# Optimization experiments

Measured on AMD Instinct MI355X. Metric: run time of the kernel, lower is better.

The kernel has to match this reference:

```python
import jax, jax.numpy as jnp
import numpy as np

B, T, D, H = 4, 4096, 1024, 64

def setup_inputs() -> dict:
    key = jax.random.key(0)
    k1, k2, k3, k4 = jax.random.split(key, 4)
    x = jax.random.normal(k1, (B, T, D), dtype=jnp.float32)
    Wk = jax.random.normal(k2, (D, H), dtype=jnp.float32) * (D ** -0.5)
    Wq = jax.random.normal(k3, (D, H), dtype=jnp.float32) * (D ** -0.5)
    Wv = jax.random.normal(k4, (D, H), dtype=jnp.float32) * (D ** -0.5)
    return {"x": x, "Wk": Wk, "Wq": Wq, "Wv": Wv}

def reference(x, Wk, Wq, Wv):
    # single-head causal self-attention (dropout inactive: training=False)
    k = x @ Wk  # [B,T,H]
    q = x @ Wq  # [B,T,H]
    v = x @ Wv  # [B,T,H]
    scale = jnp.float32(1.0) / jnp.sqrt(jnp.float32(H))
    wei = jnp.einsum('bth,bsh->bts', q, k) * scale  # [B,T,T]
    t = x.shape[1]
    causal = jnp.tril(jnp.ones((t, t), dtype=bool))[None, :, :]
    wei = jnp.where(causal, wei, jnp.float32(-jnp.inf))
    wei = jax.nn.softmax(wei, axis=-1)
    out = jnp.einsum('bts,bsh->bth', wei, v)  # [B,T,H]
    return out
```

## Files before the change

### kernel.cpp

```cpp
#include <hip/hip_runtime.h>

typedef __bf16 bf16_t;
typedef __bf16 bf16x8 __attribute__((ext_vector_type(8)));
typedef __bf16 bf16x4 __attribute__((ext_vector_type(4)));
typedef float  f32x4  __attribute__((ext_vector_type(4)));
typedef float  f32x16 __attribute__((ext_vector_type(16)));

#define B_  4
#define T_  4096
#define H_  64
#define BT  (B_*T_)

#define QSCALE 0.1803368801111204f

#define NSLOT_PB 1088
#define NSLOT    4352

#define WS_KFR  0x0000000u
#define WS_QFR  0x0200000u
#define WS_VFR  0x0400000u
#define WS_WTF  0x0600000u
#define WS_POUT 0x0680000u
#define WS_PL   0x1780000u

#define MFMA16(a,b,c) __builtin_amdgcn_mfma_f32_16x16x32_bf16((a),(b),(c),0,0,0)
#define MFMA32(a,b,c) __builtin_amdgcn_mfma_f32_32x32x16_bf16((a),(b),(c),0,0,0)

__device__ __forceinline__ unsigned pk2(float a, float b) {
  union { __bf16 h[2]; unsigned u; } u_;
  u_.h[0] = (__bf16)a; u_.h[1] = (__bf16)b;
  return u_.u;
}

__device__ __forceinline__ f32x16 zero16() {
  f32x16 z;
#pragma unroll
  for (int i = 0; i < 16; ++i) z[i] = 0.f;
  return z;
}

__global__ __launch_bounds__(128) void wtrans_kernel(
    const float* __restrict__ Wk, const float* __restrict__ Wq,
    const float* __restrict__ Wv, bf16_t* __restrict__ WTf) {
  __shared__ float lw[64][17];
  int bid = blockIdx.x;
  int nt = bid >> 4;
  int kc = bid & 15;
  int w  = nt >> 2;
  const float* W = (w == 0) ? Wk : (w == 1) ? Wq : Wv;
  float sc = (w == 1) ? QSCALE : 1.0f;
  int nl0 = (nt & 3) * 16;

  int t = threadIdx.x;
  int rr = t >> 1;
  int c0 = (t & 1) * 8;
  const float* src = W + (size_t)(kc*64 + rr)*64 + nl0 + c0;
  float4 v0 = *reinterpret_cast<const float4*>(src);
  float4 v1 = *reinterpret_cast<const float4*>(src + 4);
  lw[rr][c0+0] = v0.x; lw[rr][c0+1] = v0.y; lw[rr][c0+2] = v0.z; lw[rr][c0+3] = v0.w;
  lw[rr][c0+4] = v1.x; lw[rr][c0+5] = v1.y; lw[rr][c0+6] = v1.z; lw[rr][c0+7] = v1.w;
  __syncthreads();

  int kk   = t >> 6;
  int lane = t & 63;
  int col  = lane & 15;
  int g    = lane >> 4;
  bf16x8 o;
#pragma unroll
  for (int e = 0; e < 8; ++e) o[e] = (bf16_t)(lw[kk*32 + g*8 + e][col] * sc);
  *reinterpret_cast<bf16x8*>(WTf + ((size_t)bid*2 + kk)*512 + lane*8) = o;
}

__global__ __launch_bounds__(256) void proj_kernel(
    const float* __restrict__ x, const bf16_t* __restrict__ WTf,
    bf16_t* __restrict__ kfr, bf16_t* __restrict__ qfr, bf16_t* __restrict__ vfr) {
  __shared__ __bf16 xs[2][16][72];
  int tid  = threadIdx.x;
  int wv   = tid >> 6;
  int lane = tid & 63;
  int col  = lane & 15;
  int g    = lane >> 4;
  int m0   = blockIdx.x * 16;

  f32x4 zero4 = {0.f, 0.f, 0.f, 0.f};
  f32x4 acc[3] = {zero4, zero4, zero4};

  int srow = tid >> 4;
  int scol = (tid & 15) * 4;
  const float* xrow = x + (size_t)(m0 + srow)*1024 + scol;

  float4 a0 = *reinterpret_cast<const float4*>(xrow);
  float4 b0 = *reinterpret_cast<const float4*>(xrow + 64);
  {
    bf16x4 pk = { (bf16_t)a0.x,(bf16_t)a0.y,(bf16_t)a0.z,(bf16_t)a0.w };
    *reinterpret_cast<bf16x4*>(&xs[0][srow][scol]) = pk;
  }

  const bf16_t* wtb = WTf + lane*8;

  for (int t = 0; t < 16; ++t) {
    __syncthreads();
    int cur = t & 1;
    if (t + 2 < 16) {
      const float* p = xrow + (t+2)*64;
      if ((t & 1) == 0) a0 = *reinterpret_cast<const float4*>(p);
      else              b0 = *reinterpret_cast<const float4*>(p);
    }
#pragma unroll
    for (int kk = 0; kk < 2; ++kk) {
      int ko = kk*32 + g*8;
      bf16x8 f0 = *(const bf16x8*)&xs[cur][col][ko];
#pragma unroll
      for (int nti = 0; nti < 3; ++nti) {
        int nt = wv*3 + nti;
        bf16x8 bfr = *(const bf16x8*)(wtb + ((size_t)(nt*16 + t)*2 + kk)*512);
        acc[nti] = MFMA16(f0, bfr, acc[nti]);
      }
    }
    if (t + 1 < 16) {
      float4 sv = ((t & 1) == 0) ? b0 : a0;
      bf16x4 pk = { (bf16_t)sv.x,(bf16_t)sv.y,(bf16_t)sv.z,(bf16_t)sv.w };
      *reinterpret_cast<bf16x4*>(&xs[cur^1][srow][scol]) = pk;
    }
  }
  int row0 = m0 + 4*g;
#pragma unroll
  for (int nti = 0; nti < 3; ++nti) {
    int n = wv*48 + nti*16 + col;
    f32x4 v = acc[nti];
    if (n < 128) {
      int h = n & 63;
      bf16_t* base = (n < 64) ? kfr : qfr;
#pragma unroll
      for (int r = 0; r < 4; ++r) {
        int t2 = row0 + r;
        size_t idx = (size_t)((t2>>6)*8 + ((t2>>5)&1)*4 + (h>>4))*512
                   + (size_t)((t2&31) + ((h>>3)&1)*32)*8 + (h&7);
        base[idx] = (bf16_t)v[r];
      }
    } else {
      int h = n - 128;
      size_t idx = (size_t)((row0>>6)*8 + ((h>>5)&1)*4 + ((row0>>4)&3))*512
                 + (size_t)((h&31) + ((row0>>3)&1)*32)*8 + (row0&7);
      bf16x4 pk = { (bf16_t)v[0], (bf16_t)v[1], (bf16_t)v[2], (bf16_t)v[3] };
      *reinterpret_cast<bf16x4*>(&vfr[idx]) = pk;
    }
  }
}

__global__ __launch_bounds__(64) void attn_kernel(
    const bf16_t* __restrict__ qfr, const bf16_t* __restrict__ kfr,
    const bf16_t* __restrict__ vfr, bf16_t* __restrict__ pout,
    float* __restrict__ pl) {
  int l  = threadIdx.x;
  int ql = l & 31;
  int hi = l >> 5;

  int bidx = blockIdx.x;
  int b = bidx / NSLOT_PB;
  int s = bidx - b * NSLOT_PB;
  s = NSLOT_PB - 1 - s;
  int a = 0;
#pragma unroll
  for (int aa = 1; aa < 16; ++aa) if (4*aa*(aa+1) <= s) a = aa;
  int r2 = s - 4*a*(a+1);
  int qd = r2 / (a+1);
  int c  = r2 - qd*(a+1);
  int jt = 8*a + qd;
  int slot = b*NSLOT_PB + s;

  int q0    = jt << 5;
  int kv_lo = c << 8;
  int kv_hi = min(kv_lo + 256, q0 + 32);
  int ntiles = (kv_hi - kv_lo + 63) >> 6;
  int qg = q0 + ql;

  const bf16_t* qb = qfr + (size_t)((b*T_ + q0) >> 6)*4096
                   + (size_t)((q0 >> 5) & 1)*2048 + l*8;
  bf16x8 qf0 = *(const bf16x8*)(qb);
  bf16x8 qf1 = *(const bf16x8*)(qb + 512);
  bf16x8 qf2 = *(const bf16x8*)(qb + 1024);
  bf16x8 qf3 = *(const bf16x8*)(qb + 1536);

  const bf16_t* kfb = kfr + (size_t)(b*T_)*64 + l*8;
  const bf16_t* vfb = vfr + (size_t)(b*T_)*64 + l*8;

  bf16x8 kA0,kA1,kA2,kA3, kB0,kB1,kB2,kB3;
#define LOADK(kvt_) do { const bf16_t* kp_ = kfb + (size_t)(kvt_)*64;          \
    kA0=*(const bf16x8*)(kp_);        kA1=*(const bf16x8*)(kp_+512);           \
    kA2=*(const bf16x8*)(kp_+1024);   kA3=*(const bf16x8*)(kp_+1536);          \
    kB0=*(const bf16x8*)(kp_+2048);   kB1=*(const bf16x8*)(kp_+2560);          \
    kB2=*(const bf16x8*)(kp_+3072);   kB3=*(const bf16x8*)(kp_+3584); } while(0)

  LOADK(kv_lo);

  f32x16 oA = zero16(), oB = zero16();
  float l_ = 0.f;

  for (int t = 0; t < ntiles; ++t) {
    int kvt = kv_lo + t*64;
    const bf16_t* vp = vfb + (size_t)kvt*64;
    bf16x8 vA0 = *(const bf16x8*)(vp);
    bf16x8 vA1 = *(const bf16x8*)(vp + 512);
    bf16x8 vA2 = *(const bf16x8*)(vp + 1024);
    bf16x8 vA3 = *(const bf16x8*)(vp + 1536);
    bf16x8 vB0 = *(const bf16x8*)(vp + 2048);
    bf16x8 vB1 = *(const bf16x8*)(vp + 2560);
    bf16x8 vB2 = *(const bf16x8*)(vp + 3072);
    bf16x8 vB3 = *(const bf16x8*)(vp + 3584);

    f32x16 sA = zero16(), sB = zero16();
    __builtin_amdgcn_s_setprio(1);
    sA = MFMA32(kA0, qf0, sA); sB = MFMA32(kB0, qf0, sB);
    sA = MFMA32(kA1, qf1, sA); sB = MFMA32(kB1, qf1, sB);
    sA = MFMA32(kA2, qf2, sA); sB = MFMA32(kB2, qf2, sB);
    sA = MFMA32(kA3, qf3, sA); sB = MFMA32(kB3, qf3, sB);
    __builtin_amdgcn_s_setprio(0);

    if (t + 1 < ntiles) LOADK(kvt + 64);

    if (kvt + 63 > q0) {
#pragma unroll
      for (int r = 0; r < 16; ++r) {
        int kvo = kvt + (r&3) + 8*(r>>2) + 4*hi;
        if (kvo > qg)      sA[r] = -1e30f;
        if (kvo + 32 > qg) sB[r] = -1e30f;
      }
    }

    float pA[16], pB[16];
    float ts = 0.f;
#pragma unroll
    for (int r = 0; r < 16; ++r) { pA[r] = exp2f(sA[r]); ts += pA[r]; }
#pragma unroll
    for (int r = 0; r < 16; ++r) { pB[r] = exp2f(sB[r]); ts += pB[r]; }
    l_ += ts + __shfl_xor(ts, 32);

    bf16x8 p0, p1, p2, p3;
#define MKSLICES(P, F0, F1) do {                                               \
    unsigned w0 = pk2(P[0],P[1]),   w1 = pk2(P[2],P[3]);                       \
    unsigned w2 = pk2(P[4],P[5]),   w3 = pk2(P[6],P[7]);                       \
    unsigned w4 = pk2(P[8],P[9]),   w5 = pk2(P[10],P[11]);                     \
    unsigned w6 = pk2(P[12],P[13]), w7 = pk2(P[14],P[15]);                     \
    unsigned x0 = (unsigned)__shfl_xor((int)w0,32);                            \
    unsigned x1 = (unsigned)__shfl_xor((int)w1,32);                            \
    unsigned x2 = (unsigned)__shfl_xor((int)w2,32);                            \
    unsigned x3 = (unsigned)__shfl_xor((int)w3,32);                            \
    unsigned x4 = (unsigned)__shfl_xor((int)w4,32);                            \
    unsigned x5 = (unsigned)__shfl_xor((int)w5,32);                            \
    unsigned x6 = (unsigned)__shfl_xor((int)w6,32);                            \
    unsigned x7 = (unsigned)__shfl_xor((int)w7,32);                            \
    union { unsigned d[4]; bf16x8 v; } u0_, u1_;                               \
    u0_.d[0] = hi ? x2 : w0;  u0_.d[1] = hi ? x3 : w1;                         \
    u0_.d[2] = hi ? w2 : x0;  u0_.d[3] = hi ? w3 : x1;                         \
    u1_.d[0] = hi ? x6 : w4;  u1_.d[1] = hi ? x7 : w5;                         \
    u1_.d[2] = hi ? w6 : x4;  u1_.d[3] = hi ? w7 : x5;                         \
    F0 = u0_.v; F1 = u1_.v; } while(0)
    MKSLICES(pA, p0, p1);
    MKSLICES(pB, p2, p3);

    __builtin_amdgcn_s_setprio(1);
    oA = MFMA32(vA0, p0, oA); oB = MFMA32(vB0, p0, oB);
    oA = MFMA32(vA1, p1, oA); oB = MFMA32(vB1, p1, oB);
    oA = MFMA32(vA2, p2, oA); oB = MFMA32(vB2, p2, oB);
    oA = MFMA32(vA3, p3, oA); oB = MFMA32(vB3, p3, oB);
    __builtin_amdgcn_s_setprio(0);
  }

  bf16_t* po = pout + (size_t)slot * 2048;
#pragma unroll
  for (int r = 0; r < 16; ++r) {
    int h = (r&3) + 8*(r>>2) + 4*hi;
    po[h*32 + ql]      = (bf16_t)oA[r];
    po[(h+32)*32 + ql] = (bf16_t)oB[r];
  }
  if (l < 32) pl[(size_t)slot*32 + l] = l_;
}

__global__ __launch_bounds__(256) void combine_kernel(
    const bf16_t* __restrict__ pout, const float* __restrict__ pl,
    float* __restrict__ out) {
  int blk = blockIdx.x;
  int b  = blk >> 7;
  int jt = blk & 127;
  int tid = threadIdx.x;
  int wv = tid >> 6;
  int l  = tid & 63;
  int a  = jt >> 3;
  int nch = a + 1;
  int slot0 = b*NSLOT_PB + 4*a*(a+1) + (jt & 7)*(a+1);

  float oacc[8], lacc[8];
#pragma unroll
  for (int q = 0; q < 8; ++q) { oacc[q] = 0.f; lacc[q] = 0.f; }
  for (int c2 = 0; c2 < nch; ++c2) {
    const bf16_t* pp = pout + (size_t)(slot0 + c2)*2048 + l*32 + wv*8;
    bf16x8 o8 = *(const bf16x8*)pp;
    const float* plc = pl + (size_t)(slot0 + c2)*32 + wv*8;
#pragma unroll
    for (int q = 0; q < 8; ++q) { oacc[q] += (float)o8[q]; lacc[q] += plc[q]; }
  }
  float* op = out + ((size_t)b*T_ + (size_t)jt*32 + wv*8)*64 + l;
#pragma unroll
  for (int q = 0; q < 8; ++q) op[(size_t)q*64] = oacc[q] / lacc[q];
}

extern "C" void kernel_launch(void* const* d_in, const int* in_sizes, int n_in,
                              void* d_out, int out_size, void* d_ws, size_t ws_size,
                              hipStream_t stream) {
  (void)in_sizes; (void)n_in; (void)out_size; (void)ws_size;
  const float* x  = (const float*)d_in[0];
  const float* Wk = (const float*)d_in[1];
  const float* Wq = (const float*)d_in[2];
  const float* Wv = (const float*)d_in[3];
  char* ws = (char*)d_ws;
  bf16_t* kfr  = (bf16_t*)(ws + WS_KFR);
  bf16_t* qfr  = (bf16_t*)(ws + WS_QFR);
  bf16_t* vfr  = (bf16_t*)(ws + WS_VFR);
  bf16_t* WTf  = (bf16_t*)(ws + WS_WTF);
  bf16_t* pout = (bf16_t*)(ws + WS_POUT);
  float*  pl   = (float*)(ws + WS_PL);
  float*  outp = (float*)d_out;

  hipLaunchKernelGGL(wtrans_kernel,  dim3(192),   dim3(128), 0, stream, Wk, Wq, Wv, WTf);
  hipLaunchKernelGGL(proj_kernel,    dim3(1024),  dim3(256), 0, stream, x, WTf, kfr, qfr, vfr);
  hipLaunchKernelGGL(attn_kernel,    dim3(NSLOT), dim3(64),  0, stream, qfr, kfr, vfr, pout, pl);
  hipLaunchKernelGGL(combine_kernel, dim3(512),   dim3(256), 0, stream, pout, pl, outp);
}
```

Measured before the change: 65.57 us.

## Drop LDS staging in projection, load x directly into MFMA fragments with 32-row tiles

The projection kernel no longer stages x through shared memory with barriers. Each lane now loads its own fp32 x fragment from global memory, converts it to bf16 in registers, and feeds it to the MFMA. Each block covers 32 rows instead of 16, so every weight fragment is reused for two M-tiles, and the grid is halved. Loads are software-pipelined with even/odd register sets. The cost is that all four waves read x redundantly, relying on cache, and register pressure goes up.

```diff
diff --git a/kernel.cpp b/kernel.cpp
--- a/kernel.cpp
+++ b/kernel.cpp
@@ -74,76 +74,95 @@
 __global__ __launch_bounds__(256) void proj_kernel(
     const float* __restrict__ x, const bf16_t* __restrict__ WTf,
     bf16_t* __restrict__ kfr, bf16_t* __restrict__ qfr, bf16_t* __restrict__ vfr) {
-  __shared__ __bf16 xs[2][16][72];
   int tid  = threadIdx.x;
   int wv   = tid >> 6;
   int lane = tid & 63;
   int col  = lane & 15;
   int g    = lane >> 4;
-  int m0   = blockIdx.x * 16;
-
-  f32x4 zero4 = {0.f, 0.f, 0.f, 0.f};
-  f32x4 acc[3] = {zero4, zero4, zero4};
-
-  int srow = tid >> 4;
-  int scol = (tid & 15) * 4;
-  const float* xrow = x + (size_t)(m0 + srow)*1024 + scol;
-
-  float4 a0 = *reinterpret_cast<const float4*>(xrow);
-  float4 b0 = *reinterpret_cast<const float4*>(xrow + 64);
-  {
-    bf16x4 pk = { (bf16_t)a0.x,(bf16_t)a0.y,(bf16_t)a0.z,(bf16_t)a0.w };
-    *reinterpret_cast<bf16x4*>(&xs[0][srow][scol]) = pk;
-  }
-
-  const bf16_t* wtb = WTf + lane*8;
-
-  for (int t = 0; t < 16; ++t) {
-    __syncthreads();
-    int cur = t & 1;
-    if (t + 2 < 16) {
-      const float* p = xrow + (t+2)*64;
-      if ((t & 1) == 0) a0 = *reinterpret_cast<const float4*>(p);
-      else              b0 = *reinterpret_cast<const float4*>(p);
+  int m0   = blockIdx.x * 32;
+
+  f32x4 acc00 = {0.f,0.f,0.f,0.f}, acc01 = acc00, acc02 = acc00;
+  f32x4 acc10 = acc00, acc11 = acc00, acc12 = acc00;
+
+  const float*  xpA = x + (size_t)(m0 + col)*1024 + g*8;
+  const float*  xpB = xpA + (size_t)16*1024;
+  const bf16_t* wtb = WTf + (size_t)(wv*3)*32*512 + lane*8;
+
+  float4 aE0 = *(const float4*)(xpA);      float4 aE1 = *(const float4*)(xpA + 4);
+  float4 aE2 = *(const float4*)(xpB);      float4 aE3 = *(const float4*)(xpB + 4);
+  bf16x8 bE0 = *(const bf16x8*)(wtb + (size_t)(0*32 + 0)*512);
+  bf16x8 bE1 = *(const bf16x8*)(wtb + (size_t)(1*32 + 0)*512);
+  bf16x8 bE2 = *(const bf16x8*)(wtb + (size_t)(2*32 + 0)*512);
+  float4 aO0 = *(const float4*)(xpA + 32); float4 aO1 = *(const float4*)(xpA + 36);
+  float4 aO2 = *(const float4*)(xpB + 32); float4 aO3 = *(const float4*)(xpB + 36);
+  bf16x8 bO0 = *(const bf16x8*)(wtb + (size_t)(0*32 + 1)*512);
+  bf16x8 bO1 = *(const bf16x8*)(wtb + (size_t)(1*32 + 1)*512);
+  bf16x8 bO2 = *(const bf16x8*)(wtb + (size_t)(2*32 + 1)*512);
+
+  for (int u = 0; u < 16; ++u) {
+    {
+      bf16x8 af0 = { (bf16_t)aE0.x,(bf16_t)aE0.y,(bf16_t)aE0.z,(bf16_t)aE0.w,
+                     (bf16_t)aE1.x,(bf16_t)aE1.y,(bf16_t)aE1.z,(bf16_t)aE1.w };
+      bf16x8 af1 = { (bf16_t)aE2.x,(bf16_t)aE2.y,(bf16_t)aE2.z,(bf16_t)aE2.w,
+                     (bf16_t)aE3.x,(bf16_t)aE3.y,(bf16_t)aE3.z,(bf16_t)aE3.w };
+      bf16x8 b0 = bE0, b1 = bE1, b2 = bE2;
+      if (u < 15) {
+        int jn = 2*u + 2;
+        aE0 = *(const float4*)(xpA + jn*32);  aE1 = *(const float4*)(xpA + jn*32 + 4);
+        aE2 = *(const float4*)(xpB + jn*32);  aE3 = *(const float4*)(xpB + jn*32 + 4);
+        bE0 = *(const bf16x8*)(wtb + (size_t)(0*32 + jn)*512);
+        bE1 = *(const bf16x8*)(wtb + (size_t)(1*32 + jn)*512);
+        bE2 = *(const bf16x8*)(wtb + (size_t)(2*32 + jn)*512);
+      }
+      acc00 = MFMA16(af0, b0, acc00);  acc10 = MFMA16(af1, b0, acc10);
+      acc01 = MFMA16(af0, b1, acc01);  acc11 = MFMA16(af1, b1, acc11);
+      acc02 = MFMA16(af0, b2, acc02);  acc12 = MFMA16(af1, b2, acc12);
     }
-#pragma unroll
-    for (int kk = 0; kk < 2; ++kk) {
-      int ko = kk*32 + g*8;
-      bf16x8 f0 = *(const bf16x8*)&xs[cur][col][ko];
-#pragma unroll
-      for (int nti = 0; nti < 3; ++nti) {
-        int nt = wv*3 + nti;
-        bf16x8 bfr = *(const bf16x8*)(wtb + ((size_t)(nt*16 + t)*2 + kk)*512);
-        acc[nti] = MFMA16(f0, bfr, acc[nti]);
+    {
+      bf16x8 af0 = { (bf16_t)aO0.x,(bf16_t)aO0.y,(bf16_t)aO0.z,(bf16_t)aO0.w,
+                     (bf16_t)aO1.x,(bf16_t)aO1.y,(bf16_t)aO1.z,(bf16_t)aO1.w };
+      bf16x8 af1 = { (bf16_t)aO2.x,(bf16_t)aO2.y,(bf16_t)aO2.z,(bf16_t)aO2.w,
+                     (bf16_t)aO3.x,(bf16_t)aO3.y,(bf16_t)aO3.z,(bf16_t)aO3.w };
+      bf16x8 b0 = bO0, b1 = bO1, b2 = bO2;
+      if (u < 15) {
+        int jn = 2*u + 3;
+        aO0 = *(const float4*)(xpA + jn*32);  aO1 = *(const float4*)(xpA + jn*32 + 4);
+        aO2 = *(const float4*)(xpB + jn*32);  aO3 = *(const float4*)(xpB + jn*32 + 4);
+        bO0 = *(const bf16x8*)(wtb + (size_t)(0*32 + jn)*512);
+        bO1 = *(const bf16x8*)(wtb + (size_t)(1*32 + jn)*512);
+        bO2 = *(const bf16x8*)(wtb + (size_t)(2*32 + jn)*512);
       }
+      acc00 = MFMA16(af0, b0, acc00);  acc10 = MFMA16(af1, b0, acc10);
+      acc01 = MFMA16(af0, b1, acc01);  acc11 = MFMA16(af1, b1, acc11);
+      acc02 = MFMA16(af0, b2, acc02);  acc12 = MFMA16(af1, b2, acc12);
     }
-    if (t + 1 < 16) {
-      float4 sv = ((t & 1) == 0) ? b0 : a0;
-      bf16x4 pk = { (bf16_t)sv.x,(bf16_t)sv.y,(bf16_t)sv.z,(bf16_t)sv.w };
-      *reinterpret_cast<bf16x4*>(&xs[cur^1][srow][scol]) = pk;
-    }
-  }
-  int row0 = m0 + 4*g;
-#pragma unroll
-  for (int nti = 0; nti < 3; ++nti) {
-    int n = wv*48 + nti*16 + col;
-    f32x4 v = acc[nti];
-    if (n < 128) {
-      int h = n & 63;
-      bf16_t* base = (n < 64) ? kfr : qfr;
-#pragma unroll
-      for (int r = 0; r < 4; ++r) {
-        int t2 = row0 + r;
-        size_t idx = (size_t)((t2>>6)*8 + ((t2>>5)&1)*4 + (h>>4))*512
-                   + (size_t)((t2&31) + ((h>>3)&1)*32)*8 + (h&7);
-        base[idx] = (bf16_t)v[r];
+  }
+
+#pragma unroll
+  for (int mt = 0; mt < 2; ++mt) {
+    int row0 = m0 + mt*16 + 4*g;
+#pragma unroll
+    for (int nti = 0; nti < 3; ++nti) {
+      int n = wv*48 + nti*16 + col;
+      f32x4 v = (mt == 0) ? (nti == 0 ? acc00 : nti == 1 ? acc01 : acc02)
+                          : (nti == 0 ? acc10 : nti == 1 ? acc11 : acc12);
+      if (n < 128) {
+        int h = n & 63;
+        bf16_t* base = (n < 64) ? kfr : qfr;
+#pragma unroll
+        for (int r = 0; r < 4; ++r) {
+          int t2 = row0 + r;
+          size_t idx = (size_t)((t2>>6)*8 + ((t2>>5)&1)*4 + (h>>4))*512
+                     + (size_t)((t2&31) + ((h>>3)&1)*32)*8 + (h&7);
+          base[idx] = (bf16_t)v[r];
+        }
+      } else {
+        int h = n - 128;
+        size_t idx = (size_t)((row0>>6)*8 + ((h>>5)&1)*4 + ((row0>>4)&3))*512
+                   + (size_t)((h&31) + ((row0>>3)&1)*32)*8 + (row0&7);
+        bf16x4 pk = { (bf16_t)v[0], (bf16_t)v[1], (bf16_t)v[2], (bf16_t)v[3] };
+        *reinterpret_cast<bf16x4*>(&vfr[idx]) = pk;
       }
-    } else {
-      int h = n - 128;
-      size_t idx = (size_t)((row0>>6)*8 + ((h>>5)&1)*4 + ((row0>>4)&3))*512
-                 + (size_t)((h&31) + ((row0>>3)&1)*32)*8 + (row0&7);
-      bf16x4 pk = { (bf16_t)v[0], (bf16_t)v[1], (bf16_t)v[2], (bf16_t)v[3] };
-      *reinterpret_cast<bf16x4*>(&vfr[idx]) = pk;
     }
   }
 }
@@ -323,7 +342,7 @@
   float*  outp = (float*)d_out;
 
   hipLaunchKernelGGL(wtrans_kernel,  dim3(192),   dim3(128), 0, stream, Wk, Wq, Wv, WTf);
-  hipLaunchKernelGGL(proj_kernel,    dim3(1024),  dim3(256), 0, stream, x, WTf, kfr, qfr, vfr);
+  hipLaunchKernelGGL(proj_kernel,    dim3(512),   dim3(256), 0, stream, x, WTf, kfr, qfr, vfr);
   hipLaunchKernelGGL(attn_kernel,    dim3(NSLOT), dim3(64),  0, stream, qfr, kfr, vfr, pout, pl);
   hipLaunchKernelGGL(combine_kernel, dim3(512),   dim3(256), 0, stream, pout, pl, outp);
 }
```

New measurement: 78.84 us. +20.2%, slower.

## Rework projection kernel with direct global-to-LDS loads and 32-row tiles

Applied to the files above, without the earlier changes.

The projection kernel now stages fp32 x tiles straight into LDS with global_load_lds in a swizzled layout, replacing the register-prefetch, convert and store path. Each block now covers 32 rows instead of 16, and each wave computes a 16x96 output tile (6 MFMA accumulators), so every weight fragment is reused across more rows and only half as many blocks are launched. The goal is less register and VALU overhead plus more weight reuse. In exchange the double buffering is gone: each k-chunk waits on two barriers with no overlap between loads and MFMA work, and the bf16 conversion now happens after the LDS read.

```diff
diff --git a/kernel.cpp b/kernel.cpp
--- a/kernel.cpp
+++ b/kernel.cpp
@@ -25,6 +25,10 @@
 
 #define MFMA16(a,b,c) __builtin_amdgcn_mfma_f32_16x16x32_bf16((a),(b),(c),0,0,0)
 #define MFMA32(a,b,c) __builtin_amdgcn_mfma_f32_32x32x16_bf16((a),(b),(c),0,0,0)
+
+#define GLD16(gptr, lptr) __builtin_amdgcn_global_load_lds( \
+    (const __attribute__((address_space(1))) unsigned int*)(gptr), \
+    (__attribute__((address_space(3))) unsigned int*)(lptr), 16, 0, 0)
 
 __device__ __forceinline__ unsigned pk2(float a, float b) {
   union { __bf16 h[2]; unsigned u; } u_;
@@ -74,60 +78,70 @@
 __global__ __launch_bounds__(256) void proj_kernel(
     const float* __restrict__ x, const bf16_t* __restrict__ WTf,
     bf16_t* __restrict__ kfr, bf16_t* __restrict__ qfr, bf16_t* __restrict__ vfr) {
-  __shared__ __bf16 xs[2][16][72];
+  __shared__ __align__(16) char xsb[8192];
   int tid  = threadIdx.x;
   int wv   = tid >> 6;
   int lane = tid & 63;
   int col  = lane & 15;
   int g    = lane >> 4;
-  int m0   = blockIdx.x * 16;
-
-  f32x4 zero4 = {0.f, 0.f, 0.f, 0.f};
-  f32x4 acc[3] = {zero4, zero4, zero4};
-
-  int srow = tid >> 4;
-  int scol = (tid & 15) * 4;
-  const float* xrow = x + (size_t)(m0 + srow)*1024 + scol;
-
-  float4 a0 = *reinterpret_cast<const float4*>(xrow);
-  float4 b0 = *reinterpret_cast<const float4*>(xrow + 64);
-  {
-    bf16x4 pk = { (bf16_t)a0.x,(bf16_t)a0.y,(bf16_t)a0.z,(bf16_t)a0.w };
-    *reinterpret_cast<bf16x4*>(&xs[0][srow][scol]) = pk;
-  }
-
-  const bf16_t* wtb = WTf + lane*8;
-
-  for (int t = 0; t < 16; ++t) {
+  int wr   = wv >> 1;
+  int wc   = wv & 1;
+  int m0   = blockIdx.x * 32;
+
+  int r_lo = wv*4 + (lane >> 4);
+  int cb   = (lane & 15) * 16;
+  const char* xc = (const char*)x + (size_t)m0*4096;
+
+  f32x4 acc0 = {0.f,0.f,0.f,0.f};
+  f32x4 acc1 = acc0, acc2 = acc0, acc3 = acc0, acc4 = acc0, acc5 = acc0;
+
+  const bf16_t* wtb = WTf + (size_t)(wc*6)*32*512 + lane*8;
+
+  int rr  = wr*16 + col;
+  int sw  = (rr & 7) << 4;
+  const char* arow = xsb + rr*256;
+
+  for (int kc = 0; kc < 16; ++kc) {
     __syncthreads();
-    int cur = t & 1;
-    if (t + 2 < 16) {
-      const float* p = xrow + (t+2)*64;
-      if ((t & 1) == 0) a0 = *reinterpret_cast<const float4*>(p);
-      else              b0 = *reinterpret_cast<const float4*>(p);
+    {
+      int row0 = r_lo;
+      GLD16(xc + (size_t)row0*4096 + kc*256 + (cb ^ ((row0 & 7) << 4)),
+            xsb + wv*1024);
+      int row1 = 16 + r_lo;
+      GLD16(xc + (size_t)row1*4096 + kc*256 + (cb ^ ((row1 & 7) << 4)),
+            xsb + 4096 + wv*1024);
     }
+    __syncthreads();
+
 #pragma unroll
     for (int kk = 0; kk < 2; ++kk) {
-      int ko = kk*32 + g*8;
-      bf16x8 f0 = *(const bf16x8*)&xs[cur][col][ko];
-#pragma unroll
-      for (int nti = 0; nti < 3; ++nti) {
-        int nt = wv*3 + nti;
-        bf16x8 bfr = *(const bf16x8*)(wtb + ((size_t)(nt*16 + t)*2 + kk)*512);
-        acc[nti] = MFMA16(f0, bfr, acc[nti]);
-      }
+      int jj = kc*2 + kk;
+      int ob = kk*128 + g*32;
+      float4 lo = *reinterpret_cast<const float4*>(arow + ((ob     ) ^ sw));
+      float4 hi = *reinterpret_cast<const float4*>(arow + ((ob + 16) ^ sw));
+      bf16x8 af = { (bf16_t)lo.x,(bf16_t)lo.y,(bf16_t)lo.z,(bf16_t)lo.w,
+                    (bf16_t)hi.x,(bf16_t)hi.y,(bf16_t)hi.z,(bf16_t)hi.w };
+      bf16x8 b0 = *(const bf16x8*)(wtb + ((size_t)(0*32 + jj))*512);
+      bf16x8 b1 = *(const bf16x8*)(wtb + ((size_t)(1*32 + jj))*512);
+      bf16x8 b2 = *(const bf16x8*)(wtb + ((size_t)(2*32 + jj))*512);
+      bf16x8 b3 = *(const bf16x8*)(wtb + ((size_t)(3*32 + jj))*512);
+      bf16x8 b4 = *(const bf16x8*)(wtb + ((size_t)(4*32 + jj))*512);
+      bf16x8 b5 = *(const bf16x8*)(wtb + ((size_t)(5*32 + jj))*512);
+      acc0 = MFMA16(af, b0, acc0);
+      acc1 = MFMA16(af, b1, acc1);
+      acc2 = MFMA16(af, b2, acc2);
+      acc3 = MFMA16(af, b3, acc3);
+      acc4 = MFMA16(af, b4, acc4);
+      acc5 = MFMA16(af, b5, acc5);
     }
-    if (t + 1 < 16) {
-      float4 sv = ((t & 1) == 0) ? b0 : a0;
-      bf16x4 pk = { (bf16_t)sv.x,(bf16_t)sv.y,(bf16_t)sv.z,(bf16_t)sv.w };
-      *reinterpret_cast<bf16x4*>(&xs[cur^1][srow][scol]) = pk;
-    }
-  }
-  int row0 = m0 + 4*g;
-#pragma unroll
-  for (int nti = 0; nti < 3; ++nti) {
-    int n = wv*48 + nti*16 + col;
-    f32x4 v = acc[nti];
+  }
+
+  int row0 = m0 + wr*16 + 4*g;
+#pragma unroll
+  for (int nti = 0; nti < 6; ++nti) {
+    int n = wc*96 + nti*16 + col;
+    f32x4 v = (nti == 0) ? acc0 : (nti == 1) ? acc1 : (nti == 2) ? acc2
+            : (nti == 3) ? acc3 : (nti == 4) ? acc4 : acc5;
     if (n < 128) {
       int h = n & 63;
       bf16_t* base = (n < 64) ? kfr : qfr;
@@ -323,7 +337,7 @@
   float*  outp = (float*)d_out;
 
   hipLaunchKernelGGL(wtrans_kernel,  dim3(192),   dim3(128), 0, stream, Wk, Wq, Wv, WTf);
-  hipLaunchKernelGGL(proj_kernel,    dim3(1024),  dim3(256), 0, stream, x, WTf, kfr, qfr, vfr);
+  hipLaunchKernelGGL(proj_kernel,    dim3(512),   dim3(256), 0, stream, x, WTf, kfr, qfr, vfr);
   hipLaunchKernelGGL(attn_kernel,    dim3(NSLOT), dim3(64),  0, stream, qfr, kfr, vfr, pout, pl);
   hipLaunchKernelGGL(combine_kernel, dim3(512),   dim3(256), 0, stream, pout, pl, outp);
 }
```

After: 68.06 us. 1.04x slower.

## Stage projection input via direct global-to-LDS loads and pack attention slots four per block

Applied to the files above, without the earlier changes.

The projection kernel now copies the whole 16x1024 fp32 x tile into 64KB of LDS with global_load_lds using an XOR swizzle. It then runs a 32-step MFMA loop that converts to bf16 on read, replacing the double-buffered register staging loop and its per-step barriers. The attention kernel groups four independent work slots into one 256-thread block instead of launching 64-thread blocks. The large LDS footprint limits projection occupancy to about two blocks per CU, and fp32 staging doubles the LDS traffic.

```diff
diff --git a/kernel.cpp b/kernel.cpp
--- a/kernel.cpp
+++ b/kernel.cpp
@@ -25,6 +25,10 @@
 
 #define MFMA16(a,b,c) __builtin_amdgcn_mfma_f32_16x16x32_bf16((a),(b),(c),0,0,0)
 #define MFMA32(a,b,c) __builtin_amdgcn_mfma_f32_32x32x16_bf16((a),(b),(c),0,0,0)
+
+#define GLD16(gptr, lptr) __builtin_amdgcn_global_load_lds( \
+    (const __attribute__((address_space(1))) unsigned int*)(gptr), \
+    (__attribute__((address_space(3))) unsigned int*)(lptr), 16, 0, 0)
 
 __device__ __forceinline__ unsigned pk2(float a, float b) {
   union { __bf16 h[2]; unsigned u; } u_;
@@ -74,7 +78,7 @@
 __global__ __launch_bounds__(256) void proj_kernel(
     const float* __restrict__ x, const bf16_t* __restrict__ WTf,
     bf16_t* __restrict__ kfr, bf16_t* __restrict__ qfr, bf16_t* __restrict__ vfr) {
-  __shared__ __bf16 xs[2][16][72];
+  __shared__ __align__(16) char xsb[65536];
   int tid  = threadIdx.x;
   int wv   = tid >> 6;
   int lane = tid & 63;
@@ -82,52 +86,39 @@
   int g    = lane >> 4;
   int m0   = blockIdx.x * 16;
 
-  f32x4 zero4 = {0.f, 0.f, 0.f, 0.f};
-  f32x4 acc[3] = {zero4, zero4, zero4};
-
-  int srow = tid >> 4;
-  int scol = (tid & 15) * 4;
-  const float* xrow = x + (size_t)(m0 + srow)*1024 + scol;
-
-  float4 a0 = *reinterpret_cast<const float4*>(xrow);
-  float4 b0 = *reinterpret_cast<const float4*>(xrow + 64);
-  {
-    bf16x4 pk = { (bf16_t)a0.x,(bf16_t)a0.y,(bf16_t)a0.z,(bf16_t)a0.w };
-    *reinterpret_cast<bf16x4*>(&xs[0][srow][scol]) = pk;
-  }
-
-  const bf16_t* wtb = WTf + lane*8;
-
-  for (int t = 0; t < 16; ++t) {
-    __syncthreads();
-    int cur = t & 1;
-    if (t + 2 < 16) {
-      const float* p = xrow + (t+2)*64;
-      if ((t & 1) == 0) a0 = *reinterpret_cast<const float4*>(p);
-      else              b0 = *reinterpret_cast<const float4*>(p);
-    }
-#pragma unroll
-    for (int kk = 0; kk < 2; ++kk) {
-      int ko = kk*32 + g*8;
-      bf16x8 f0 = *(const bf16x8*)&xs[cur][col][ko];
-#pragma unroll
-      for (int nti = 0; nti < 3; ++nti) {
-        int nt = wv*3 + nti;
-        bf16x8 bfr = *(const bf16x8*)(wtb + ((size_t)(nt*16 + t)*2 + kk)*512);
-        acc[nti] = MFMA16(f0, bfr, acc[nti]);
-      }
-    }
-    if (t + 1 < 16) {
-      float4 sv = ((t & 1) == 0) ? b0 : a0;
-      bf16x4 pk = { (bf16_t)sv.x,(bf16_t)sv.y,(bf16_t)sv.z,(bf16_t)sv.w };
-      *reinterpret_cast<bf16x4*>(&xs[cur^1][srow][scol]) = pk;
-    }
-  }
+  const char* xgs = (const char*)x + (size_t)m0*4096;
+  int csw = wv*1024 + lane*16;
+#pragma unroll
+  for (int i = 0; i < 16; ++i)
+    GLD16(xgs + (size_t)i*4096 + (csw ^ ((i & 7) << 5)),
+          xsb + i*4096 + wv*1024);
+  __syncthreads();
+
+  f32x4 acc0 = {0.f,0.f,0.f,0.f}, acc1 = acc0, acc2 = acc0;
+  const bf16_t* wtb = WTf + (size_t)(wv*3)*32*512 + lane*8;
+  const char* arow = xsb + (size_t)col*4096;
+  int sw = (col & 7) << 5;
+
+#pragma unroll 4
+  for (int j = 0; j < 32; ++j) {
+    int ob = j*128 + g*32;
+    float4 lo = *reinterpret_cast<const float4*>(arow + ((ob     ) ^ sw));
+    float4 hi = *reinterpret_cast<const float4*>(arow + ((ob + 16) ^ sw));
+    bf16x8 af = { (bf16_t)lo.x,(bf16_t)lo.y,(bf16_t)lo.z,(bf16_t)lo.w,
+                  (bf16_t)hi.x,(bf16_t)hi.y,(bf16_t)hi.z,(bf16_t)hi.w };
+    bf16x8 b0 = *(const bf16x8*)(wtb + ((size_t)(0*32 + j))*512);
+    bf16x8 b1 = *(const bf16x8*)(wtb + ((size_t)(1*32 + j))*512);
+    bf16x8 b2 = *(const bf16x8*)(wtb + ((size_t)(2*32 + j))*512);
+    acc0 = MFMA16(af, b0, acc0);
+    acc1 = MFMA16(af, b1, acc1);
+    acc2 = MFMA16(af, b2, acc2);
+  }
+
   int row0 = m0 + 4*g;
 #pragma unroll
   for (int nti = 0; nti < 3; ++nti) {
     int n = wv*48 + nti*16 + col;
-    f32x4 v = acc[nti];
+    f32x4 v = (nti == 0) ? acc0 : (nti == 1) ? acc1 : acc2;
     if (n < 128) {
       int h = n & 63;
       bf16_t* base = (n < 64) ? kfr : qfr;
@@ -148,17 +139,19 @@
   }
 }
 
-__global__ __launch_bounds__(64) void attn_kernel(
+__global__ __launch_bounds__(256) void attn_kernel(
     const bf16_t* __restrict__ qfr, const bf16_t* __restrict__ kfr,
     const bf16_t* __restrict__ vfr, bf16_t* __restrict__ pout,
     float* __restrict__ pl) {
-  int l  = threadIdx.x;
-  int ql = l & 31;
-  int hi = l >> 5;
-
-  int bidx = blockIdx.x;
-  int b = bidx / NSLOT_PB;
-  int s = bidx - b * NSLOT_PB;
+  int tid = threadIdx.x;
+  int wv  = tid >> 6;
+  int l   = tid & 63;
+  int ql  = l & 31;
+  int hi  = l >> 5;
+
+  int si = blockIdx.x * 4 + wv;
+  int b = si / NSLOT_PB;
+  int s = si - b * NSLOT_PB;
   s = NSLOT_PB - 1 - s;
   int a = 0;
 #pragma unroll
@@ -324,6 +317,6 @@
 
   hipLaunchKernelGGL(wtrans_kernel,  dim3(192),   dim3(128), 0, stream, Wk, Wq, Wv, WTf);
   hipLaunchKernelGGL(proj_kernel,    dim3(1024),  dim3(256), 0, stream, x, WTf, kfr, qfr, vfr);
-  hipLaunchKernelGGL(attn_kernel,    dim3(NSLOT), dim3(64),  0, stream, qfr, kfr, vfr, pout, pl);
+  hipLaunchKernelGGL(attn_kernel,    dim3(1088),  dim3(256), 0, stream, qfr, kfr, vfr, pout, pl);
   hipLaunchKernelGGL(combine_kernel, dim3(512),   dim3(256), 0, stream, pout, pl, outp);
 }
```

Result: slower. 67.69 us (+3.2%).
